# Performance work log

Hardware: AMD Instinct MI355X
Metric: run time of the kernel (lower is better)

## Reference

```python
import jax, jax.numpy as jnp
import numpy as np
import math

NUM_HEADS = 16
HEAD_SIZE = 64
HIDDEN = NUM_HEADS * HEAD_SIZE
LN_EPS = 1e-12


def setup_inputs() -> dict:
    key = jax.random.key(0)
    ks = jax.random.split(key, 8)
    B, Lw, Le, H = 8, 512, 64, HIDDEN
    scale = 0.02
    return {
        "word_hidden_states": jax.random.normal(ks[0], (B, Lw, H), jnp.float32),
        "entity_hidden_states": jax.random.normal(ks[1], (B, Le, H), jnp.float32),
        "attention_mask": jnp.zeros((B, 1, 1, Lw + Le), jnp.float32),
        "Wq": jax.random.normal(ks[2], (H, H), jnp.float32) * scale,
        "bq": jnp.zeros((H,), jnp.float32),
        "Wk": jax.random.normal(ks[3], (H, H), jnp.float32) * scale,
        "bk": jnp.zeros((H,), jnp.float32),
        "Wv": jax.random.normal(ks[4], (H, H), jnp.float32) * scale,
        "bv": jnp.zeros((H,), jnp.float32),
        "Wo": jax.random.normal(ks[5], (H, H), jnp.float32) * scale,
        "bo": jnp.zeros((H,), jnp.float32),
        "ln_w": jnp.ones((H,), jnp.float32),
        "ln_b": jnp.zeros((H,), jnp.float32),
    }


def _layernorm(x, w, b):
    u = jnp.mean(x, axis=-1, keepdims=True)
    s = jnp.mean(jnp.square(x - u), axis=-1, keepdims=True)
    return w * ((x - u) / jnp.sqrt(s + LN_EPS)) + b


def reference(word_hidden_states, entity_hidden_states, attention_mask,
              Wq, bq, Wk, bk, Wv, bv, Wo, bo, ln_w, ln_b):
    B, Lw, H = word_hidden_states.shape
    x = jnp.concatenate([word_hidden_states, entity_hidden_states], axis=1)  # [B,S,H]
    S = x.shape[1]

    def heads(t):  # [B,S,H] -> [B,nh,S,hd]
        return t.reshape(B, S, NUM_HEADS, HEAD_SIZE).transpose(0, 2, 1, 3)

    q = heads(x @ Wq + bq)
    k = heads(x @ Wk + bk)
    v = heads(x @ Wv + bv)

    scores = jnp.einsum("bhqd,bhkd->bhqk", q, k) / math.sqrt(HEAD_SIZE)
    scores = scores + attention_mask  # additive mask, broadcast [B,1,1,S]
    probs = jax.nn.softmax(scores, axis=-1)
    ctx = jnp.einsum("bhqk,bhkd->bhqd", probs, v)
    ctx = ctx.transpose(0, 2, 1, 3).reshape(B, S, H)

    # SelfOutput (shared weights) applied per-stream; equivalent on concat since
    # residual is the concatenated input and LayerNorm is per-token.
    out = _layernorm(ctx @ Wo + bo + x, ln_w, ln_b)
    return out[:, :Lw, :], out[:, Lw:, :]
```

## Files before the change

kernel.cpp:

```cpp
#include <hip/hip_runtime.h>

#define NHEADS 16
#define HDIM   64
#define HID    1024
#define BATCH  8
#define LW     512
#define LE     64
#define SEQ    576
#define MTOT   (BATCH * SEQ)

typedef unsigned short u16;
typedef __bf16 bf16x8 __attribute__((ext_vector_type(8)));
typedef float  f32x4  __attribute__((ext_vector_type(4)));

__device__ __forceinline__ u16 f2bf(float f) {
  union { float f; unsigned int i; } x;
  x.f = f;
  unsigned int u = x.i;
  unsigned int r = (u + 0x7FFFu + ((u >> 16) & 1u)) >> 16;
  return (u16)r;
}
__device__ __forceinline__ unsigned int pk2(float a, float b) {
  return (unsigned int)f2bf(a) | ((unsigned int)f2bf(b) << 16);
}

__device__ __forceinline__ void gload16(const u16* g, u16* l) {
  __builtin_amdgcn_global_load_lds(
      (const __attribute__((address_space(1))) void*)g,
      (__attribute__((address_space(3))) void*)l, 16, 0, 0);
}

__global__ __launch_bounds__(256) void prep_k(
    const float* __restrict__ w0, const float* __restrict__ w1,
    const float* __restrict__ w2, const float* __restrict__ w3,
    u16* __restrict__ wt,
    const float* __restrict__ word, const float* __restrict__ ent,
    u16* __restrict__ xb)
{
  const int bid = blockIdx.x, tid = threadIdx.x;
  if (bid < 4096) {
    __shared__ u16 tile[32][33];
    const int z = bid >> 10, rem = bid & 1023;
    const int bx = rem & 31, by = rem >> 5;
    const float* src = (z == 0) ? w0 : (z == 1) ? w1 : (z == 2) ? w2 : w3;
    u16* dst = wt + (size_t)z * HID * HID;
    const int tx = tid & 31, ty = tid >> 5;
    const int nx = bx * 32, ky = by * 32;
#pragma unroll
    for (int j = 0; j < 4; ++j)
      tile[ty * 4 + j][tx] = f2bf(src[(size_t)(ky + ty * 4 + j) * HID + nx + tx]);
    __syncthreads();
#pragma unroll
    for (int j = 0; j < 4; ++j)
      dst[(size_t)(nx + ty * 4 + j) * HID + ky + tx] = tile[tx][ty * 4 + j];
  } else {
    const int row = bid - 4096;
    const int bb = row / SEQ, ss = row - bb * SEQ;
    const float* src = (ss < LW) ? word + (size_t)(bb * LW + ss) * HID
                                 : ent  + (size_t)(bb * LE + (ss - LW)) * HID;
    float4 v = *(const float4*)(src + tid * 4);
    ushort4 o;
    o.x = f2bf(v.x); o.y = f2bf(v.y); o.z = f2bf(v.z); o.w = f2bf(v.w);
    *(ushort4*)(xb + (size_t)row * HID + tid * 4) = o;
  }
}

#define Q_MFMA(AF, BF, H, NB)                                                 \
  if (which < 2) {                                                            \
    _Pragma("unroll")                                                         \
    for (int mi = 0; mi < 4; ++mi)                                            \
      _Pragma("unroll")                                                       \
      for (int nj = 0; nj < 2; ++nj)                                          \
        _Pragma("unroll")                                                     \
        for (int ks = 0; ks < 2; ++ks)                                        \
          acc[(H)*4 + (NB) + nj][mi] = __builtin_amdgcn_mfma_f32_16x16x32_bf16( \
              BF[nj][ks], AF[mi][ks], acc[(H)*4 + (NB) + nj][mi], 0, 0, 0);   \
  } else {                                                                    \
    _Pragma("unroll")                                                         \
    for (int mi = 0; mi < 4; ++mi)                                            \
      _Pragma("unroll")                                                       \
      for (int nj = 0; nj < 2; ++nj)                                          \
        _Pragma("unroll")                                                     \
        for (int ks = 0; ks < 2; ++ks)                                        \
          acc[(H)*4 + mi][(NB) + nj] = __builtin_amdgcn_mfma_f32_16x16x32_bf16( \
              AF[mi][ks], BF[nj][ks], acc[(H)*4 + mi][(NB) + nj], 0, 0, 0);   \
  }

__global__ __launch_bounds__(512, 2) void qkv_gemm_k(
    const u16* __restrict__ xb, const u16* __restrict__ wt,
    const float* __restrict__ bq, const float* __restrict__ bk, const float* __restrict__ bv,
    u16* __restrict__ q_ws, u16* __restrict__ k_ws, u16* __restrict__ v_ws)
{
  __shared__ u16 sh[65536];
  const int which = blockIdx.z;
  const u16* W = wt + (size_t)which * HID * HID;
  const float* bias = (which == 0) ? bq : (which == 1) ? bk : bv;
  const int m0 = blockIdx.x * 256, n0 = blockIdx.y * 256;
  const int tid = threadIdx.x, lane = tid & 63, wv = tid >> 6;
  const int lr = lane & 15, quad = lane >> 4;
  const int wm = (wv >> 2) * 128, wn = (wv & 3) * 64;
  const int fsw = lr & 7;
  const int k0o = ((quad ^ fsw)) * 8;
  const int k1o = (((4 + quad) ^ fsw)) * 8;
  const int aCh = (wv >> 2) * 8192;
  const int bCh = (wv & 3) * 4096;
  const int arow = lr * 64;

  const int srow = tid >> 3;
  const int goff = ((tid & 7) ^ (srow & 7)) * 8;
  const u16* asrc = xb + (size_t)(m0 + srow) * HID + goff;
  const u16* bsrc = W  + (size_t)(n0 + srow) * HID + goff;
  const int ldst = tid * 8;

#pragma unroll
  for (int c = 0; c < 4; ++c)
    gload16(asrc + (size_t)c * 64 * HID, sh + c * 4096 + ldst);
#pragma unroll
  for (int c = 0; c < 4; ++c)
    gload16(bsrc + (size_t)c * 64 * HID, sh + 16384 + c * 4096 + ldst);
#pragma unroll
  for (int c = 0; c < 4; ++c)
    gload16(asrc + (size_t)c * 64 * HID + 64, sh + 32768 + c * 4096 + ldst);
#pragma unroll
  for (int c = 0; c < 4; ++c)
    gload16(bsrc + (size_t)c * 64 * HID + 64, sh + 32768 + 16384 + c * 4096 + ldst);
  asm volatile("s_waitcnt vmcnt(8)" ::: "memory");
  __builtin_amdgcn_s_barrier();

  const f32x4 fz = {0.f, 0.f, 0.f, 0.f};
  f32x4 acc[8][4];
#pragma unroll
  for (int a = 0; a < 8; ++a)
#pragma unroll
    for (int b = 0; b < 4; ++b) acc[a][b] = fz;

  for (int s = 0; s < 16; ++s) {
    const int bo = (s & 1) << 15;
    u16* As = sh + bo;
    u16* Bs = sh + bo + 16384;
    const int sOff = (s + 2) * 64;
    const bool gpre = (s < 14);

    bf16x8 af[4][2], bfL[2][2], bfH[2][2];

#pragma unroll
    for (int mi = 0; mi < 4; ++mi) {
      af[mi][0] = *(const bf16x8*)(&As[aCh + mi * 1024 + arow + k0o]);
      af[mi][1] = *(const bf16x8*)(&As[aCh + mi * 1024 + arow + k1o]);
    }
#pragma unroll
    for (int nj = 0; nj < 2; ++nj) {
      bfL[nj][0] = *(const bf16x8*)(&Bs[bCh + nj * 1024 + arow + k0o]);
      bfL[nj][1] = *(const bf16x8*)(&Bs[bCh + nj * 1024 + arow + k1o]);
    }
    asm volatile("s_waitcnt lgkmcnt(8)" ::: "memory");
    __builtin_amdgcn_s_barrier();
    asm volatile("s_waitcnt lgkmcnt(0)" ::: "memory");
    __builtin_amdgcn_sched_barrier(0);
    __builtin_amdgcn_s_setprio(1);
    Q_MFMA(af, bfL, 0, 0)
    __builtin_amdgcn_s_setprio(0);
    __builtin_amdgcn_s_barrier();

#pragma unroll
    for (int nj = 0; nj < 2; ++nj) {
      bfH[nj][0] = *(const bf16x8*)(&Bs[bCh + (2 + nj) * 1024 + arow + k0o]);
      bfH[nj][1] = *(const bf16x8*)(&Bs[bCh + (2 + nj) * 1024 + arow + k1o]);
    }
    if (gpre) {
      gload16(asrc + (size_t)0 * 64 * HID + sOff, sh + bo + 0 * 4096 + ldst);
      gload16(asrc + (size_t)2 * 64 * HID + sOff, sh + bo + 2 * 4096 + ldst);
    }
    __builtin_amdgcn_s_barrier();
    asm volatile("s_waitcnt lgkmcnt(0)" ::: "memory");
    __builtin_amdgcn_sched_barrier(0);
    __builtin_amdgcn_s_setprio(1);
    Q_MFMA(af, bfH, 0, 2)
    __builtin_amdgcn_s_setprio(0);
    __builtin_amdgcn_s_barrier();

#pragma unroll
    for (int mi = 0; mi < 4; ++mi) {
      af[mi][0] = *(const bf16x8*)(&As[aCh + 4096 + mi * 1024 + arow + k0o]);
      af[mi][1] = *(const bf16x8*)(&As[aCh + 4096 + mi * 1024 + arow + k1o]);
    }
    if (gpre) {
      gload16(bsrc + (size_t)0 * 64 * HID + sOff, sh + bo + 16384 + 0 * 4096 + ldst);
      gload16(bsrc + (size_t)1 * 64 * HID + sOff, sh + bo + 16384 + 1 * 4096 + ldst);
      gload16(bsrc + (size_t)2 * 64 * HID + sOff, sh + bo + 16384 + 2 * 4096 + ldst);
      gload16(bsrc + (size_t)3 * 64 * HID + sOff, sh + bo + 16384 + 3 * 4096 + ldst);
    }
    __builtin_amdgcn_s_barrier();
    asm volatile("s_waitcnt lgkmcnt(0)" ::: "memory");
    __builtin_amdgcn_sched_barrier(0);
    __builtin_amdgcn_s_setprio(1);
    Q_MFMA(af, bfH, 1, 2)
    __builtin_amdgcn_s_setprio(0);
    __builtin_amdgcn_s_barrier();

    if (gpre) {
      gload16(asrc + (size_t)1 * 64 * HID + sOff, sh + bo + 1 * 4096 + ldst);
      gload16(asrc + (size_t)3 * 64 * HID + sOff, sh + bo + 3 * 4096 + ldst);
    }
    __builtin_amdgcn_s_barrier();
    __builtin_amdgcn_sched_barrier(0);
    __builtin_amdgcn_s_setprio(1);
    Q_MFMA(af, bfL, 1, 0)
    __builtin_amdgcn_s_setprio(0);
    if (s < 14)       asm volatile("s_waitcnt vmcnt(8)" ::: "memory");
    else if (s == 14) asm volatile("s_waitcnt vmcnt(0)" ::: "memory");
    __builtin_amdgcn_s_barrier();
  }

  u16* tb = sh + wv * (64 * 68);
  const int head = (n0 + wn) >> 6;

  if (which < 2) {
    float4 bias4[4];
#pragma unroll
    for (int ni = 0; ni < 4; ++ni)
      bias4[ni] = *(const float4*)(bias + n0 + wn + ni * 16 + quad * 4);
    u16* qk = (which == 0 ? q_ws : k_ws);
#pragma unroll
    for (int g = 0; g < 2; ++g) {
      const int mbase = m0 + wm + g * 64;
      const int bb = mbase / SEQ;
      const int ssb = mbase - bb * SEQ;
#pragma unroll
      for (int mi = 0; mi < 4; ++mi)
#pragma unroll
        for (int ni = 0; ni < 4; ++ni) {
          const f32x4 a = acc[g * 4 + ni][mi];
          uint2 w2v;
          w2v.x = pk2(a[0] + bias4[ni].x, a[1] + bias4[ni].y);
          w2v.y = pk2(a[2] + bias4[ni].z, a[3] + bias4[ni].w);
          *(uint2*)(&tb[(mi * 16 + lr) * 68 + ni * 16 + quad * 4]) = w2v;
        }
      u16* drow = qk + ((size_t)(bb * NHEADS + head) * SEQ + ssb) * HDIM;
#pragma unroll
      for (int i = 0; i < 8; ++i) {
        int rrow = i * 8 + (lane >> 3);
        int seg = lane & 7;
        bf16x8 v8 = *(const bf16x8*)(&tb[rrow * 68 + seg * 8]);
        *(bf16x8*)(drow + (size_t)rrow * HDIM + seg * 8) = v8;
      }
    }
  } else {
    float bcol[4];
#pragma unroll
    for (int ni = 0; ni < 4; ++ni) bcol[ni] = bias[n0 + wn + ni * 16 + lr];
#pragma unroll
    for (int g = 0; g < 2; ++g) {
      const int mbase = m0 + wm + g * 64;
      const int bb = mbase / SEQ;
      const int ssb = mbase - bb * SEQ;
#pragma unroll
      for (int mi = 0; mi < 4; ++mi)
#pragma unroll
        for (int ni = 0; ni < 4; ++ni) {
          const f32x4 a = acc[g * 4 + mi][ni];
          uint2 w2v;
          w2v.x = pk2(a[0] + bcol[ni], a[1] + bcol[ni]);
          w2v.y = pk2(a[2] + bcol[ni], a[3] + bcol[ni]);
          *(uint2*)(&tb[(ni * 16 + lr) * 68 + (mi >> 1) * 32 + quad * 8 + (mi & 1) * 4]) = w2v;
        }
      u16* dcol = v_ws + ((size_t)(bb * NHEADS + head) * HDIM) * SEQ + ssb;
#pragma unroll
      for (int i = 0; i < 8; ++i) {
        int d = i * 8 + (lane >> 3);
        int seg = lane & 7;
        bf16x8 v8 = *(const bf16x8*)(&tb[d * 68 + seg * 8]);
        *(bf16x8*)(dcol + (size_t)d * SEQ + seg * 8) = v8;
      }
    }
  }
}

__global__ __launch_bounds__(256) void attn_k(
    const u16* __restrict__ q_ws, const u16* __restrict__ k_ws,
    const u16* __restrict__ v_ws, const float* __restrict__ mask,
    u16* __restrict__ ctxh)
{
  __shared__ u16 Ks[4096];
  __shared__ u16 Vs[4096];
  __shared__ float ms[576];
  const int bhx = blockIdx.x, qt = blockIdx.y;
  const int b = bhx >> 4, h = bhx & 15;
  const int tid = threadIdx.x, lane = tid & 63, wv = tid >> 6;
  const int lr = lane & 15, quad = lane >> 4;
  const int q0 = qt * 64 + wv * 16;
  const u16* kbh = k_ws + (size_t)bhx * SEQ * HDIM;
  const u16* vbh = v_ws + (size_t)bhx * HDIM * SEQ;
  const u16* qp  = q_ws + ((size_t)bhx * SEQ + q0) * HDIM;
  const float* mrow = mask + b * SEQ;

  if (tid < 144) *(float4*)(&ms[tid * 4]) = *(const float4*)(mrow + tid * 4);

  const int subrow = lane >> 3;
  const int gsw = (lane & 7) ^ subrow;

  bf16x8 qf[2];
  qf[0] = *(const bf16x8*)(qp + lr * HDIM + quad * 8);
  qf[1] = *(const bf16x8*)(qp + lr * HDIM + 32 + quad * 8);

  const f32x4 fz = {0.f, 0.f, 0.f, 0.f};
  f32x4 oa[4] = {fz, fz, fz, fz};
  f32x4 rsv = fz;
  const int fA = lr & 7;

  for (int ci = 0; ci < 9; ++ci) {
    const int c = ci * 64;
#pragma unroll
    for (int j = 0; j < 2; ++j) {
      int row = (wv * 2 + j) * 8 + subrow;
      gload16(kbh + ((size_t)(c + row)) * HDIM + gsw * 8,
              &Ks[((wv * 2 + j) * 64 + lane) * 8]);
      gload16(vbh + (size_t)row * SEQ + c + gsw * 8,
              &Vs[((wv * 2 + j) * 64 + lane) * 8]);
    }
    __syncthreads();
    f32x4 s[4] = {fz, fz, fz, fz};
#pragma unroll
    for (int ks = 0; ks < 2; ++ks)
#pragma unroll
      for (int t = 0; t < 4; ++t) {
        bf16x8 kf = *(const bf16x8*)(&Ks[(t * 16 + lr) * 64 + (((ks * 4 + quad) ^ fA) * 8)]);
        s[t] = __builtin_amdgcn_mfma_f32_16x16x32_bf16(kf, qf[ks], s[t], 0, 0, 0);
      }
    unsigned int pk0[4], pk1[4];
#pragma unroll
    for (int t = 0; t < 4; ++t) {
      float4 mv = *(const float4*)(&ms[c + t * 16 + quad * 4]);
      s[t][0] = __expf(s[t][0] * 0.125f + mv.x);
      s[t][1] = __expf(s[t][1] * 0.125f + mv.y);
      s[t][2] = __expf(s[t][2] * 0.125f + mv.z);
      s[t][3] = __expf(s[t][3] * 0.125f + mv.w);
      rsv += s[t];
      pk0[t] = pk2(s[t][0], s[t][1]);
      pk1[t] = pk2(s[t][2], s[t][3]);
    }
#pragma unroll
    for (int ks = 0; ks < 2; ++ks) {
      union { unsigned int u[4]; bf16x8 v; } ap;
      ap.u[0] = pk0[ks * 2];     ap.u[1] = pk1[ks * 2];
      ap.u[2] = pk0[ks * 2 + 1]; ap.u[3] = pk1[ks * 2 + 1];
#pragma unroll
      for (int n = 0; n < 4; ++n) {
        bf16x8 vf = *(const bf16x8*)(&Vs[(n * 16 + lr) * 64 + (((ks * 4 + quad) ^ fA) * 8)]);
        oa[n] = __builtin_amdgcn_mfma_f32_16x16x32_bf16(ap.v, vf, oa[n], 0, 0, 0);
      }
    }
    __syncthreads();
  }

  float rl = rsv[0] + rsv[1] + rsv[2] + rsv[3];
  rl += __shfl_xor(rl, 16);
  rl += __shfl_xor(rl, 32);
  float inv = 1.0f / rl;
  float invr[4];
#pragma unroll
  for (int r = 0; r < 4; ++r) invr[r] = __shfl(inv, quad * 4 + r);

  u16* pw = (wv < 2) ? &Ks[wv * 2048] : &Vs[(wv - 2) * 2048];
#pragma unroll
  for (int n = 0; n < 4; ++n)
#pragma unroll
    for (int r = 0; r < 4; ++r)
      pw[(quad * 4 + r) * 68 + n * 16 + lr] = f2bf(oa[n][r] * invr[r]);
  const int token0 = b * SEQ + q0;
  u16* cb = ctxh + ((size_t)h * MTOT + token0) * HDIM;
#pragma unroll
  for (int i = 0; i < 2; ++i) {
    int row = lane & 15;
    int seg = (lane >> 4) + i * 4;
    bf16x8 v8 = *(const bf16x8*)(&pw[row * 68 + seg * 8]);
    *(bf16x8*)(cb + (size_t)row * HDIM + seg * 8) = v8;
  }
}

__global__ __launch_bounds__(256) void out_gemm_k(
    const u16* __restrict__ ctxh, const u16* __restrict__ wto,
    const float* __restrict__ bo,
    const float* __restrict__ word, const float* __restrict__ ent,
    float* __restrict__ y)
{
  __shared__ u16 sh[10240];
  u16* As = sh;
  u16* Bs = sh + 2048;
  const int m0 = blockIdx.x * 32, n0 = blockIdx.y * 128;
  const int tid = threadIdx.x, lane = tid & 63, wv = tid >> 6;
  const int lr = lane & 15, quad = lane >> 4;
  const int wn = wv * 32;
  const int subrow = lane >> 3;
  const int gsw = ((lane & 7) ^ subrow) * 8;
  const int fsw = lr & 7;

  const f32x4 fz = {0.f, 0.f, 0.f, 0.f};
  f32x4 acc[2][2];
#pragma unroll
  for (int mi = 0; mi < 2; ++mi)
#pragma unroll
    for (int ni = 0; ni < 2; ++ni) acc[mi][ni] = fz;

  for (int hb = 0; hb < 16; ++hb) {
    {
      int row = wv * 8 + subrow;
      gload16(ctxh + ((size_t)hb * MTOT + (m0 + row)) * HDIM + gsw,
              As + (wv * 64 + lane) * 8);
    }
#pragma unroll
    for (int j = 0; j < 4; ++j) {
      int row = (wv * 4 + j) * 8 + subrow;
      gload16(wto + (size_t)(n0 + row) * HID + hb * 64 + gsw,
              Bs + ((wv * 4 + j) * 64 + lane) * 8);
    }
    __syncthreads();
#pragma unroll
    for (int ks = 0; ks < 2; ++ks) {
      const int kc = (((ks * 4 + quad) ^ fsw) * 8);
      bf16x8 af[2], bfr[2];
#pragma unroll
      for (int i = 0; i < 2; ++i) {
        af[i]  = *(const bf16x8*)(&As[(i * 16 + lr) * 64 + kc]);
        bfr[i] = *(const bf16x8*)(&Bs[(wn + i * 16 + lr) * 64 + kc]);
      }
#pragma unroll
      for (int mi = 0; mi < 2; ++mi)
#pragma unroll
        for (int ni = 0; ni < 2; ++ni)
          acc[mi][ni] = __builtin_amdgcn_mfma_f32_16x16x32_bf16(af[mi], bfr[ni], acc[mi][ni], 0, 0, 0);
    }
    __syncthreads();
  }

#pragma unroll
  for (int mi = 0; mi < 2; ++mi) {
    int rowb = m0 + mi * 16 + quad * 4;
#pragma unroll
    for (int r = 0; r < 4; ++r) {
      int row = rowb + r;
      int bb = row / SEQ, ss = row - bb * SEQ;
      const float* res = (ss < LW) ? (word + (size_t)(bb * LW + ss) * HID)
                                   : (ent  + (size_t)(bb * LE + (ss - LW)) * HID);
#pragma unroll
      for (int ni = 0; ni < 2; ++ni) {
        int col = n0 + wn + ni * 16 + lr;
        y[(size_t)row * HID + col] = acc[mi][ni][r] + bo[col] + res[col];
      }
    }
  }
}

__global__ __launch_bounds__(256) void ln_k(
    const float* __restrict__ y, const float* __restrict__ lnw,
    const float* __restrict__ lnb, float* __restrict__ out)
{
  const int row = blockIdx.x;
  const int tid = threadIdx.x;
  __shared__ float ssum[4], sqq[4];

  const float* yr = y + (size_t)row * HID;
  float4 v = *(const float4*)(yr + tid * 4);
  float s = v.x + v.y + v.z + v.w;
  float q = v.x * v.x + v.y * v.y + v.z * v.z + v.w * v.w;
#pragma unroll
  for (int o = 32; o > 0; o >>= 1) { s += __shfl_xor(s, o); q += __shfl_xor(q, o); }
  if ((tid & 63) == 0) { ssum[tid >> 6] = s; sqq[tid >> 6] = q; }
  __syncthreads();
  s = ssum[0] + ssum[1] + ssum[2] + ssum[3];
  q = sqq[0] + sqq[1] + sqq[2] + sqq[3];
  float mean = s * (1.0f / HID);
  float var  = q * (1.0f / HID) - mean * mean;
  float rstd = rsqrtf(var + 1e-12f);

  int bb = row / SEQ, ss2 = row - bb * SEQ;
  float* dst = (ss2 < LW)
             ? out + (size_t)(bb * LW + ss2) * HID
             : out + (size_t)BATCH * LW * HID + (size_t)(bb * LE + (ss2 - LW)) * HID;

  float4 w4 = *(const float4*)(lnw + tid * 4);
  float4 b4 = *(const float4*)(lnb + tid * 4);
  float4 o4;
  o4.x = w4.x * (v.x - mean) * rstd + b4.x;
  o4.y = w4.y * (v.y - mean) * rstd + b4.y;
  o4.z = w4.z * (v.z - mean) * rstd + b4.z;
  o4.w = w4.w * (v.w - mean) * rstd + b4.w;
  *(float4*)(dst + tid * 4) = o4;
}

extern "C" void kernel_launch(void* const* d_in, const int* in_sizes, int n_in,
                              void* d_out, int out_size, void* d_ws, size_t ws_size,
                              hipStream_t stream) {
  const float* word = (const float*)d_in[0];
  const float* ent  = (const float*)d_in[1];
  const float* mask = (const float*)d_in[2];
  const float* Wq   = (const float*)d_in[3];
  const float* bq   = (const float*)d_in[4];
  const float* Wk   = (const float*)d_in[5];
  const float* bk   = (const float*)d_in[6];
  const float* Wv   = (const float*)d_in[7];
  const float* bv   = (const float*)d_in[8];
  const float* Wo   = (const float*)d_in[9];
  const float* bo   = (const float*)d_in[10];
  const float* lnw  = (const float*)d_in[11];
  const float* lnb  = (const float*)d_in[12];

  char* base = (char*)d_ws;
  u16*   wt   = (u16*)base;
  u16*   q_ws = (u16*)(base + (size_t)8 * 1024 * 1024);
  u16*   k_ws = q_ws + (size_t)MTOT * HID;
  u16*   v_ws = k_ws + (size_t)MTOT * HID;
  u16*   ctxh = v_ws + (size_t)MTOT * HID;
  char*  xy   = (char*)(ctxh + (size_t)MTOT * HID);
  u16*   xb   = (u16*)xy;
  float* y    = (float*)xy;

  hipLaunchKernelGGL(prep_k, dim3(4096 + MTOT), dim3(256), 0, stream,
                     Wq, Wk, Wv, Wo, wt, word, ent, xb);
  hipLaunchKernelGGL(qkv_gemm_k, dim3(MTOT / 256, HID / 256, 3), dim3(512), 0, stream,
                     xb, wt, bq, bk, bv, q_ws, k_ws, v_ws);
  hipLaunchKernelGGL(attn_k, dim3(BATCH * NHEADS, SEQ / 64), dim3(256), 0, stream,
                     q_ws, k_ws, v_ws, mask, ctxh);
  hipLaunchKernelGGL(out_gemm_k, dim3(MTOT / 32, HID / 128), dim3(256), 0, stream,
                     ctxh, wt + (size_t)3 * HID * HID, bo, word, ent, y);
  hipLaunchKernelGGL(ln_k, dim3(MTOT), dim3(256), 0, stream,
                     y, lnw, lnb, (float*)d_out);
}
```

Baseline: 197.1 us.

## Retile weight transpose, pack rows per block, read attention K/V from global directly

Weight transposition now uses 64x64 tiles with float4 loads and 16-byte bf16 stores. The activation conversion and LayerNorm now process one row per wavefront, four rows per block, which drops the cross-wave shared-memory reduction and the barrier from LayerNorm. The attention kernel no longer stages K and V through LDS with async loads and barriers. It loads MFMA fragments straight from global memory into registers, which removes the per-chunk synchronisation but relies on cache hits and may add global traffic and latency.

```diff
diff --git a/kernel.cpp b/kernel.cpp
--- a/kernel.cpp
+++ b/kernel.cpp
@@ -38,30 +38,48 @@
     u16* __restrict__ xb)
 {
   const int bid = blockIdx.x, tid = threadIdx.x;
-  if (bid < 4096) {
-    __shared__ u16 tile[32][33];
-    const int z = bid >> 10, rem = bid & 1023;
-    const int bx = rem & 31, by = rem >> 5;
+  if (bid < 1024) {
+    __shared__ u16 tile[64][65];
+    const int z = bid >> 8, rem = bid & 255;
+    const int bx = rem & 15, by = rem >> 4;
     const float* src = (z == 0) ? w0 : (z == 1) ? w1 : (z == 2) ? w2 : w3;
     u16* dst = wt + (size_t)z * HID * HID;
-    const int tx = tid & 31, ty = tid >> 5;
-    const int nx = bx * 32, ky = by * 32;
-#pragma unroll
-    for (int j = 0; j < 4; ++j)
-      tile[ty * 4 + j][tx] = f2bf(src[(size_t)(ky + ty * 4 + j) * HID + nx + tx]);
+    const int nx = bx * 64, ky = by * 64;
+    const int lrow = tid >> 4;
+    const int lcol = (tid & 15) * 4;
+#pragma unroll
+    for (int j = 0; j < 4; ++j) {
+      const int kk = lrow + j * 16;
+      float4 v = *(const float4*)(src + (size_t)(ky + kk) * HID + nx + lcol);
+      tile[kk][lcol + 0] = f2bf(v.x);
+      tile[kk][lcol + 1] = f2bf(v.y);
+      tile[kk][lcol + 2] = f2bf(v.z);
+      tile[kk][lcol + 3] = f2bf(v.w);
+    }
     __syncthreads();
-#pragma unroll
-    for (int j = 0; j < 4; ++j)
-      dst[(size_t)(nx + ty * 4 + j) * HID + ky + tx] = tile[tx][ty * 4 + j];
+    const int orow = tid >> 2;
+    const int oseg = (tid & 3) * 16;
+    union { u16 u[16]; bf16x8 v[2]; } tt;
+#pragma unroll
+    for (int i = 0; i < 16; ++i) tt.u[i] = tile[oseg + i][orow];
+    u16* dp = dst + (size_t)(nx + orow) * HID + ky + oseg;
+    *(bf16x8*)(dp) = tt.v[0];
+    *(bf16x8*)(dp + 8) = tt.v[1];
   } else {
-    const int row = bid - 4096;
+    const int row = (bid - 1024) * 4 + (tid >> 6);
+    const int lane = tid & 63;
     const int bb = row / SEQ, ss = row - bb * SEQ;
     const float* src = (ss < LW) ? word + (size_t)(bb * LW + ss) * HID
                                  : ent  + (size_t)(bb * LE + (ss - LW)) * HID;
-    float4 v = *(const float4*)(src + tid * 4);
-    ushort4 o;
-    o.x = f2bf(v.x); o.y = f2bf(v.y); o.z = f2bf(v.z); o.w = f2bf(v.w);
-    *(ushort4*)(xb + (size_t)row * HID + tid * 4) = o;
+    u16* drow = xb + (size_t)row * HID;
+#pragma unroll
+    for (int i = 0; i < 4; ++i) {
+      const int f = i * 256 + lane * 4;
+      float4 v = *(const float4*)(src + f);
+      ushort4 o;
+      o.x = f2bf(v.x); o.y = f2bf(v.y); o.z = f2bf(v.z); o.w = f2bf(v.w);
+      *(ushort4*)(drow + f) = o;
+    }
   }
 }
 
@@ -281,9 +299,8 @@
     const u16* __restrict__ v_ws, const float* __restrict__ mask,
     u16* __restrict__ ctxh)
 {
-  __shared__ u16 Ks[4096];
-  __shared__ u16 Vs[4096];
   __shared__ float ms[576];
+  __shared__ u16 pws[4][16 * 68];
   const int bhx = blockIdx.x, qt = blockIdx.y;
   const int b = bhx >> 4, h = bhx & 15;
   const int tid = threadIdx.x, lane = tid & 63, wv = tid >> 6;
@@ -296,37 +313,33 @@
 
   if (tid < 144) *(float4*)(&ms[tid * 4]) = *(const float4*)(mrow + tid * 4);
 
-  const int subrow = lane >> 3;
-  const int gsw = (lane & 7) ^ subrow;
-
   bf16x8 qf[2];
   qf[0] = *(const bf16x8*)(qp + lr * HDIM + quad * 8);
   qf[1] = *(const bf16x8*)(qp + lr * HDIM + 32 + quad * 8);
+  __syncthreads();
 
   const f32x4 fz = {0.f, 0.f, 0.f, 0.f};
   f32x4 oa[4] = {fz, fz, fz, fz};
   f32x4 rsv = fz;
-  const int fA = lr & 7;
 
   for (int ci = 0; ci < 9; ++ci) {
     const int c = ci * 64;
-#pragma unroll
-    for (int j = 0; j < 2; ++j) {
-      int row = (wv * 2 + j) * 8 + subrow;
-      gload16(kbh + ((size_t)(c + row)) * HDIM + gsw * 8,
-              &Ks[((wv * 2 + j) * 64 + lane) * 8]);
-      gload16(vbh + (size_t)row * SEQ + c + gsw * 8,
-              &Vs[((wv * 2 + j) * 64 + lane) * 8]);
-    }
-    __syncthreads();
+    const u16* kc = kbh + (size_t)c * HDIM;
+    const u16* vc = vbh + c;
     f32x4 s[4] = {fz, fz, fz, fz};
 #pragma unroll
     for (int ks = 0; ks < 2; ++ks)
 #pragma unroll
       for (int t = 0; t < 4; ++t) {
-        bf16x8 kf = *(const bf16x8*)(&Ks[(t * 16 + lr) * 64 + (((ks * 4 + quad) ^ fA) * 8)]);
+        bf16x8 kf = *(const bf16x8*)(kc + (size_t)(t * 16 + lr) * HDIM + (ks * 4 + quad) * 8);
         s[t] = __builtin_amdgcn_mfma_f32_16x16x32_bf16(kf, qf[ks], s[t], 0, 0, 0);
       }
+    bf16x8 vfr[4][2];
+#pragma unroll
+    for (int n = 0; n < 4; ++n)
+#pragma unroll
+      for (int ks = 0; ks < 2; ++ks)
+        vfr[n][ks] = *(const bf16x8*)(vc + (size_t)(n * 16 + lr) * SEQ + (ks * 4 + quad) * 8);
     unsigned int pk0[4], pk1[4];
 #pragma unroll
     for (int t = 0; t < 4; ++t) {
@@ -345,12 +358,9 @@
       ap.u[0] = pk0[ks * 2];     ap.u[1] = pk1[ks * 2];
       ap.u[2] = pk0[ks * 2 + 1]; ap.u[3] = pk1[ks * 2 + 1];
 #pragma unroll
-      for (int n = 0; n < 4; ++n) {
-        bf16x8 vf = *(const bf16x8*)(&Vs[(n * 16 + lr) * 64 + (((ks * 4 + quad) ^ fA) * 8)]);
-        oa[n] = __builtin_amdgcn_mfma_f32_16x16x32_bf16(ap.v, vf, oa[n], 0, 0, 0);
-      }
-    }
-    __syncthreads();
+      for (int n = 0; n < 4; ++n)
+        oa[n] = __builtin_amdgcn_mfma_f32_16x16x32_bf16(ap.v, vfr[n][ks], oa[n], 0, 0, 0);
+    }
   }
 
   float rl = rsv[0] + rsv[1] + rsv[2] + rsv[3];
@@ -361,7 +371,7 @@
 #pragma unroll
   for (int r = 0; r < 4; ++r) invr[r] = __shfl(inv, quad * 4 + r);
 
-  u16* pw = (wv < 2) ? &Ks[wv * 2048] : &Vs[(wv - 2) * 2048];
+  u16* pw = pws[wv];
 #pragma unroll
   for (int n = 0; n < 4; ++n)
 #pragma unroll
@@ -455,20 +465,21 @@
     const float* __restrict__ y, const float* __restrict__ lnw,
     const float* __restrict__ lnb, float* __restrict__ out)
 {
-  const int row = blockIdx.x;
   const int tid = threadIdx.x;
-  __shared__ float ssum[4], sqq[4];
+  const int row = blockIdx.x * 4 + (tid >> 6);
+  const int lane = tid & 63;
 
   const float* yr = y + (size_t)row * HID;
-  float4 v = *(const float4*)(yr + tid * 4);
-  float s = v.x + v.y + v.z + v.w;
-  float q = v.x * v.x + v.y * v.y + v.z * v.z + v.w * v.w;
+  float4 v[4];
+  float s = 0.f, q = 0.f;
+#pragma unroll
+  for (int i = 0; i < 4; ++i) {
+    v[i] = *(const float4*)(yr + i * 256 + lane * 4);
+    s += v[i].x + v[i].y + v[i].z + v[i].w;
+    q += v[i].x * v[i].x + v[i].y * v[i].y + v[i].z * v[i].z + v[i].w * v[i].w;
+  }
 #pragma unroll
   for (int o = 32; o > 0; o >>= 1) { s += __shfl_xor(s, o); q += __shfl_xor(q, o); }
-  if ((tid & 63) == 0) { ssum[tid >> 6] = s; sqq[tid >> 6] = q; }
-  __syncthreads();
-  s = ssum[0] + ssum[1] + ssum[2] + ssum[3];
-  q = sqq[0] + sqq[1] + sqq[2] + sqq[3];
   float mean = s * (1.0f / HID);
   float var  = q * (1.0f / HID) - mean * mean;
   float rstd = rsqrtf(var + 1e-12f);
@@ -478,14 +489,18 @@
              ? out + (size_t)(bb * LW + ss2) * HID
              : out + (size_t)BATCH * LW * HID + (size_t)(bb * LE + (ss2 - LW)) * HID;
 
-  float4 w4 = *(const float4*)(lnw + tid * 4);
-  float4 b4 = *(const float4*)(lnb + tid * 4);
-  float4 o4;
-  o4.x = w4.x * (v.x - mean) * rstd + b4.x;
-  o4.y = w4.y * (v.y - mean) * rstd + b4.y;
-  o4.z = w4.z * (v.z - mean) * rstd + b4.z;
-  o4.w = w4.w * (v.w - mean) * rstd + b4.w;
-  *(float4*)(dst + tid * 4) = o4;
+#pragma unroll
+  for (int i = 0; i < 4; ++i) {
+    const int f = i * 256 + lane * 4;
+    float4 w4 = *(const float4*)(lnw + f);
+    float4 b4 = *(const float4*)(lnb + f);
+    float4 o4;
+    o4.x = w4.x * (v[i].x - mean) * rstd + b4.x;
+    o4.y = w4.y * (v[i].y - mean) * rstd + b4.y;
+    o4.z = w4.z * (v[i].z - mean) * rstd + b4.z;
+    o4.w = w4.w * (v[i].w - mean) * rstd + b4.w;
+    *(float4*)(dst + f) = o4;
+  }
 }
 
 extern "C" void kernel_launch(void* const* d_in, const int* in_sizes, int n_in,
@@ -515,7 +530,7 @@
   u16*   xb   = (u16*)xy;
   float* y    = (float*)xy;
 
-  hipLaunchKernelGGL(prep_k, dim3(4096 + MTOT), dim3(256), 0, stream,
+  hipLaunchKernelGGL(prep_k, dim3(1024 + MTOT / 4), dim3(256), 0, stream,
                      Wq, Wk, Wv, Wo, wt, word, ent, xb);
   hipLaunchKernelGGL(qkv_gemm_k, dim3(MTOT / 256, HID / 256, 3), dim3(512), 0, stream,
                      xb, wt, bq, bk, bv, q_ws, k_ws, v_ws);
@@ -523,6 +538,6 @@
                      q_ws, k_ws, v_ws, mask, ctxh);
   hipLaunchKernelGGL(out_gemm_k, dim3(MTOT / 32, HID / 128), dim3(256), 0, stream,
                      ctxh, wt + (size_t)3 * HID * HID, bo, word, ent, y);
-  hipLaunchKernelGGL(ln_k, dim3(MTOT), dim3(256), 0, stream,
+  hipLaunchKernelGGL(ln_k, dim3(MTOT / 4), dim3(256), 0, stream,
                      y, lnw, lnb, (float*)d_out);
 }
```

New measurement: 267.8 us. +35.9%, slower.
